# Performance work log

Hardware: AMD Instinct MI355X
Metric: run time of the kernel (lower is better)

## Reference

```python
import jax, jax.numpy as jnp
import numpy as np

HEADS = 16
DIM_HEAD = 64
DIM = 1024
SCALE = DIM_HEAD ** -0.5


def setup_inputs() -> dict:
    key = jax.random.key(0)
    ks = jax.random.split(key, 6)
    b, n = 1, 3072  # torch code is only shape-correct for b == 1

    def w(k, shape, fan_in):
        return jax.random.normal(k, shape, jnp.float32) * (fan_in ** -0.5)

    x = jax.random.normal(ks[0], (b, n, DIM), jnp.float32)
    Wqkv = w(ks[1], (DIM, 3 * HEADS * DIM_HEAD), DIM)          # to_qkv (no bias)
    W1 = w(ks[2], (DIM_HEAD, DIM_HEAD), DIM_HEAD)              # mlp layer 1
    b1 = jnp.zeros((DIM_HEAD,), jnp.float32)
    W2 = w(ks[3], (DIM_HEAD, 1), DIM_HEAD)                     # mlp layer 2
    b2 = jnp.zeros((1,), jnp.float32)
    Wout = w(ks[4], (HEADS * DIM_HEAD, DIM), HEADS * DIM_HEAD) # to_out
    bout = jnp.zeros((DIM,), jnp.float32)
    return {"x": x, "Wqkv": Wqkv, "W1": W1, "b1": b1, "W2": W2, "b2": b2,
            "Wout": Wout, "bout": bout}


def reference(x, Wqkv, W1, b1, W2, b2, Wout, bout):
    b, n, _ = x.shape
    qkv = x @ Wqkv                                   # [b, n, 3*h*d]
    q, k, v = jnp.split(qkv, 3, axis=-1)
    to_heads = lambda t: t.reshape(b, n, HEADS, DIM_HEAD).transpose(0, 2, 1, 3)
    q, k, v = to_heads(q), to_heads(k), to_heads(v)  # [b, h, n, d]

    dots = jnp.einsum('bhid,bhjd->bhij', q, k) * SCALE  # [b, h, n, n]

    # key spikiness MLP: Linear -> ReLU -> Linear -> Sigmoid, then softmax over n
    spiky = jax.nn.sigmoid(jnp.maximum(k @ W1 + b1, 0.0) @ W2 + b2)[..., 0]  # [b, h, n]
    spiky_weights = jax.nn.softmax(spiky, axis=-1)                            # [b, h, n]

    # For b=1 the torch broadcast reduces to a per-QUERY scaling of the logits
    weighted_dots = dots * spiky_weights[:, :, :, None]
    weights = jax.nn.softmax(weighted_dots, axis=-1)

    out = jnp.einsum('bhij,bhjd->bhid', weights, v)       # [b, h, n, d]
    out = out.transpose(0, 2, 1, 3).reshape(b, n, HEADS * DIM_HEAD)
    return out @ Wout + bout
```

## Files before the change

### kernel.cpp

```cpp
#include <hip/hip_runtime.h>
#include <hip/hip_bf16.h>
#include <math.h>

typedef __bf16 bf16_t;
typedef __bf16 bf16x8 __attribute__((ext_vector_type(8)));
typedef float floatx4 __attribute__((ext_vector_type(4)));

#define NSEQ 3072
#define QKVLD 3072
#define DMODEL 1024

__device__ inline bf16x8 load8(const float* p) {
    floatx4 a = *(const floatx4*)p;
    floatx4 b = *(const floatx4*)(p + 4);
    bf16x8 r;
    r[0] = (bf16_t)a[0]; r[1] = (bf16_t)a[1]; r[2] = (bf16_t)a[2]; r[3] = (bf16_t)a[3];
    r[4] = (bf16_t)b[0]; r[5] = (bf16_t)b[1]; r[6] = (bf16_t)b[2]; r[7] = (bf16_t)b[3];
    return r;
}

__device__ inline void gload16(const bf16_t* g, bf16_t* l) {
    __builtin_amdgcn_global_load_lds(
        (const __attribute__((address_space(1))) unsigned int*)g,
        (__attribute__((address_space(3))) unsigned int*)l, 16, 0, 0);
}

__global__ __launch_bounds__(256) void prep_kernel(const float* __restrict__ x,
                                                   const float* __restrict__ Wqkv,
                                                   const float* __restrict__ Wout,
                                                   bf16_t* __restrict__ xb,
                                                   bf16_t* __restrict__ WqkvT,
                                                   bf16_t* __restrict__ WoutT,
                                                   float* __restrict__ Mf) {
    __shared__ float T[64][65];
    const int b = blockIdx.x, tid = threadIdx.x;
    if (b < 1536) {
        int i = b * 2048 + tid * 8;
        *(bf16x8*)(xb + i) = load8(x + i);
        return;
    }
    if (b >= 2560) {
        const floatx4 z = {0.f, 0.f, 0.f, 0.f};
        if (b < 2576) {
            floatx4* p = (floatx4*)(Mf + (b - 2560) * 4096);
#pragma unroll
            for (int i = 0; i < 4; ++i) p[i * 256 + tid] = z;
        } else {
            float* zp = Mf + 65536;
            for (int i = tid; i < 2064; i += 256) zp[i] = 0.f;
        }
        return;
    }
    const float* in; bf16_t* out; int K, N, bx, by;
    if (b < 2304) { int l = b - 1536; bx = l % 48; by = l / 48; in = Wqkv; out = WqkvT; K = 1024; N = 3072; }
    else          { int l = b - 2304; bx = l & 15; by = l >> 4; in = Wout; out = WoutT; K = 1024; N = 1024; }
    const int n0 = bx * 64, k0 = by * 64;
    const int r = tid >> 2, c0 = (tid & 3) * 16;
#pragma unroll
    for (int i = 0; i < 4; ++i) {
        floatx4 v = *(const floatx4*)(in + (size_t)(k0 + r) * N + n0 + c0 + i * 4);
        T[r][c0 + i * 4 + 0] = v[0]; T[r][c0 + i * 4 + 1] = v[1];
        T[r][c0 + i * 4 + 2] = v[2]; T[r][c0 + i * 4 + 3] = v[3];
    }
    __syncthreads();
    bf16x8 o0, o1;
#pragma unroll
    for (int i = 0; i < 8; ++i) { o0[i] = (bf16_t)T[c0 + i][r]; o1[i] = (bf16_t)T[c0 + 8 + i][r]; }
    *(bf16x8*)(out + (size_t)(n0 + r) * K + k0 + c0)     = o0;
    *(bf16x8*)(out + (size_t)(n0 + r) * K + k0 + c0 + 8) = o1;
}

template <int TN, typename CT>
__global__ __launch_bounds__(256) void gemm_bt(const bf16_t* __restrict__ A,
                                               const bf16_t* __restrict__ BT,
                                               const float* __restrict__ bias,
                                               CT* __restrict__ C,
                                               int M, int N, int K) {
    constexpr int MI = (TN == 128) ? 4 : 2;
    __shared__ __attribute__((aligned(16))) bf16_t As[128 * 64];
    __shared__ __attribute__((aligned(16))) bf16_t Bs[TN * 64];
    const int tid = threadIdx.x;
    const int wave = tid >> 6, lane = tid & 63;
    const int lr = lane & 15, quad = lane >> 4;
    const int wr = (TN == 128) ? (wave >> 1) * 64 : wave * 32;
    const int wc = (TN == 128) ? (wave & 1) * 64 : 0;
    const int m0 = blockIdx.y * 128, n0 = blockIdx.x * TN;
    const int srow = lane >> 3;
    const int schunk = (lane & 7) ^ srow;

    const floatx4 fzero = {0.f, 0.f, 0.f, 0.f};
    floatx4 acc[MI][4];
#pragma unroll
    for (int mi = 0; mi < MI; ++mi)
#pragma unroll
        for (int ni = 0; ni < 4; ++ni) acc[mi][ni] = fzero;

    for (int kb = 0; kb < K; kb += 64) {
        __syncthreads();
#pragma unroll
        for (int it = 0; it < 4; ++it) {
            const int r0 = (wave * 4 + it) * 8;
            gload16(A + (size_t)(m0 + r0 + srow) * K + kb + schunk * 8, &As[r0 * 64]);
        }
#pragma unroll
        for (int it = 0; it < TN / 32; ++it) {
            const int r0 = (wave * (TN / 32) + it) * 8;
            gload16(BT + (size_t)(n0 + r0 + srow) * K + kb + schunk * 8, &Bs[r0 * 64]);
        }
        __syncthreads();
#pragma unroll
        for (int ch = 0; ch < 2; ++ch) {
            bf16x8 af[MI], bfr[4];
#pragma unroll
            for (int mi = 0; mi < MI; ++mi)
                af[mi] = *(const bf16x8*)(&As[(wr + mi * 16 + lr) * 64 + (((ch * 4 + quad) ^ (lr & 7)) * 8)]);
#pragma unroll
            for (int ni = 0; ni < 4; ++ni)
                bfr[ni] = *(const bf16x8*)(&Bs[(wc + ni * 16 + lr) * 64 + (((ch * 4 + quad) ^ (lr & 7)) * 8)]);
#pragma unroll
            for (int mi = 0; mi < MI; ++mi)
#pragma unroll
                for (int ni = 0; ni < 4; ++ni)
                    acc[mi][ni] = __builtin_amdgcn_mfma_f32_16x16x32_bf16(af[mi], bfr[ni], acc[mi][ni], 0, 0, 0);
        }
    }

#pragma unroll
    for (int mi = 0; mi < MI; ++mi)
#pragma unroll
        for (int ni = 0; ni < 4; ++ni) {
            int n = n0 + wc + ni * 16 + lr;
            float bv = bias ? bias[n] : 0.f;
#pragma unroll
            for (int r = 0; r < 4; ++r) {
                int m = m0 + wr + mi * 16 + quad * 4 + r;
                C[(size_t)m * N + n] = (CT)(acc[mi][ni][r] + bv);
            }
        }
}

__global__ __launch_bounds__(256) void prep2_kernel(const bf16_t* __restrict__ qkv,
                                                    const float* __restrict__ W1,
                                                    const float* __restrict__ b1,
                                                    const float* __restrict__ W2,
                                                    const float* __restrict__ b2,
                                                    float* __restrict__ sfull,
                                                    float* __restrict__ hsum,
                                                    float* __restrict__ Mf,
                                                    float* __restrict__ Ksumf,
                                                    float* __restrict__ Vsumf) {
    __shared__ __attribute__((aligned(16))) bf16_t Kt[64][72];
    __shared__ __attribute__((aligned(16))) bf16_t Vt[64][72];
    __shared__ float W1s[64][65];
    __shared__ float W2s[64], b1s[64];
    const int b = blockIdx.x, tid = threadIdx.x;
    if (b < 192) {
        const int h = b / 12, j = (b % 12) * 256 + tid;
        for (int i = tid; i < 4096; i += 256) W1s[i >> 6][i & 63] = W1[i];
        if (tid < 64) { W2s[tid] = W2[tid]; b1s[tid] = b1[tid]; }
        __syncthreads();
        float kv[64];
        const bf16x8* kp8 = (const bf16x8*)(qkv + (size_t)j * QKVLD + DMODEL + h * 64);
#pragma unroll
        for (int c = 0; c < 8; ++c) {
            bf16x8 v = kp8[c];
#pragma unroll
            for (int ii = 0; ii < 8; ++ii) kv[c * 8 + ii] = (float)v[ii];
        }
        float s = b2[0];
        for (int dd = 0; dd < 64; ++dd) {
            float a = b1s[dd];
#pragma unroll
            for (int d = 0; d < 64; ++d) a += kv[d] * W1s[d][dd];
            a = fmaxf(a, 0.f);
            s += a * W2s[dd];
        }
        s = 1.f / (1.f + __expf(-s));
        sfull[h * NSEQ + j] = s;
        float e = __expf(s);
#pragma unroll
        for (int off = 1; off < 64; off <<= 1) e += __shfl_xor(e, off, 64);
        if ((tid & 63) == 0) atomicAdd(&hsum[h], e);
    } else {
        const int l = b - 192;
        const int h = l / 12, c = l % 12;
        const int wave = tid >> 6, lane = tid & 63;
        const int lr = lane & 15, quad = lane >> 4;
        const int jj = tid >> 3, ch = (tid & 7) * 8;
        const floatx4 fzero = {0.f, 0.f, 0.f, 0.f};
        floatx4 macc[4];
#pragma unroll
        for (int ni = 0; ni < 4; ++ni) macc[ni] = fzero;
        float ksum = 0.f, vsum = 0.f;

        for (int st = 0; st < 4; ++st) {
            const size_t row0 = (size_t)(c * 256 + st * 64);
            bf16x8 k0 = *(const bf16x8*)(qkv + (row0 + jj) * QKVLD + DMODEL + h * 64 + ch);
            bf16x8 k1 = *(const bf16x8*)(qkv + (row0 + jj + 32) * QKVLD + DMODEL + h * 64 + ch);
            bf16x8 v0 = *(const bf16x8*)(qkv + (row0 + jj) * QKVLD + 2 * DMODEL + h * 64 + ch);
            bf16x8 v1 = *(const bf16x8*)(qkv + (row0 + jj + 32) * QKVLD + 2 * DMODEL + h * 64 + ch);
            __syncthreads();
#pragma unroll
            for (int ii = 0; ii < 8; ++ii) {
                Kt[ch + ii][jj] = k0[ii]; Kt[ch + ii][jj + 32] = k1[ii];
                Vt[ch + ii][jj] = v0[ii]; Vt[ch + ii][jj + 32] = v1[ii];
            }
            __syncthreads();
            bf16x8 a0 = *(const bf16x8*)(&Kt[wave * 16 + lr][quad * 8]);
            bf16x8 a1 = *(const bf16x8*)(&Kt[wave * 16 + lr][32 + quad * 8]);
#pragma unroll
            for (int ni = 0; ni < 4; ++ni) {
                bf16x8 b0 = *(const bf16x8*)(&Vt[ni * 16 + lr][quad * 8]);
                bf16x8 b1f = *(const bf16x8*)(&Vt[ni * 16 + lr][32 + quad * 8]);
                macc[ni] = __builtin_amdgcn_mfma_f32_16x16x32_bf16(a0, b0, macc[ni], 0, 0, 0);
                macc[ni] = __builtin_amdgcn_mfma_f32_16x16x32_bf16(a1, b1f, macc[ni], 0, 0, 0);
            }
            if (tid < 64) {
#pragma unroll
                for (int cc = 0; cc < 8; ++cc) {
                    bf16x8 kk = *(const bf16x8*)(&Kt[tid][cc * 8]);
#pragma unroll
                    for (int ii = 0; ii < 8; ++ii) ksum += (float)kk[ii];
                }
            } else if (tid < 128) {
                const int d = tid - 64;
#pragma unroll
                for (int cc = 0; cc < 8; ++cc) {
                    bf16x8 vv = *(const bf16x8*)(&Vt[d][cc * 8]);
#pragma unroll
                    for (int ii = 0; ii < 8; ++ii) vsum += (float)vv[ii];
                }
            }
        }
        float* mh = Mf + (size_t)h * 4096;
#pragma unroll
        for (int ni = 0; ni < 4; ++ni)
#pragma unroll
            for (int r = 0; r < 4; ++r)
                atomicAdd(&mh[(wave * 16 + quad * 4 + r) * 64 + ni * 16 + lr], macc[ni][r]);
        if (tid < 64) atomicAdd(&Ksumf[h * 64 + tid], ksum);
        else if (tid < 128) atomicAdd(&Vsumf[h * 64 + (tid - 64)], vsum);
    }
}

__global__ __launch_bounds__(256) void mid_kernel(const bf16_t* __restrict__ qkv,
                                                  const bf16_t* __restrict__ WoutT,
                                                  const float* __restrict__ Mf,
                                                  const float* __restrict__ Ksumf,
                                                  const float* __restrict__ Vsumf,
                                                  const float* __restrict__ sfull,
                                                  const float* __restrict__ hsum,
                                                  bf16_t* __restrict__ Gt,
                                                  bf16_t* __restrict__ Qt) {
    const int b = blockIdx.x, tid = threadIdx.x;
    if (b < 128) {
        __shared__ __attribute__((aligned(16))) bf16_t Ms[64][72];
        __shared__ float Vss[64];
        const int h = b >> 3, ot = b & 7;
        for (int i = tid; i < 4096; i += 256)
            Ms[i >> 6][i & 63] = (bf16_t)Mf[(size_t)h * 4096 + i];
        if (tid < 64) Vss[tid] = Vsumf[h * 64 + tid];
        __syncthreads();

        const int wave = tid >> 6, lane = tid & 63;
        const int lr = lane & 15, quad = lane >> 4;
        const floatx4 fzero = {0.f, 0.f, 0.f, 0.f};
        floatx4 acc[2][4];
#pragma unroll
        for (int mi = 0; mi < 2; ++mi)
#pragma unroll
            for (int ni = 0; ni < 4; ++ni) acc[mi][ni] = fzero;
#pragma unroll
        for (int chk = 0; chk < 2; ++chk) {
            bf16x8 af[2], bfr[4];
#pragma unroll
            for (int mi = 0; mi < 2; ++mi) {
                const int o = ot * 128 + wave * 32 + mi * 16 + lr;
                af[mi] = *(const bf16x8*)(WoutT + (size_t)o * 1024 + h * 64 + chk * 32 + quad * 8);
            }
#pragma unroll
            for (int ni = 0; ni < 4; ++ni)
                bfr[ni] = *(const bf16x8*)(&Ms[ni * 16 + lr][chk * 32 + quad * 8]);
#pragma unroll
            for (int mi = 0; mi < 2; ++mi)
#pragma unroll
                for (int ni = 0; ni < 4; ++ni)
                    acc[mi][ni] = __builtin_amdgcn_mfma_f32_16x16x32_bf16(af[mi], bfr[ni], acc[mi][ni], 0, 0, 0);
        }
#pragma unroll
        for (int mi = 0; mi < 2; ++mi)
#pragma unroll
            for (int ni = 0; ni < 4; ++ni)
#pragma unroll
                for (int r = 0; r < 4; ++r) {
                    const int o = ot * 128 + wave * 32 + mi * 16 + quad * 4 + r;
                    Gt[(size_t)o * 1088 + h * 64 + ni * 16 + lr] = (bf16_t)acc[mi][ni][r];
                }
        if (tid < 128) {
            const int o = ot * 128 + tid;
            float u = 0.f;
            const bf16x8* wp = (const bf16x8*)(WoutT + (size_t)o * 1024 + h * 64);
#pragma unroll
            for (int cc = 0; cc < 8; ++cc) {
                bf16x8 w = wp[cc];
#pragma unroll
                for (int ii = 0; ii < 8; ++ii) u += (float)w[ii] * Vss[cc * 8 + ii];
            }
            Gt[(size_t)o * 1088 + 1024 + h] = (bf16_t)u;
            if (h == 0) {
                const bf16x8 bz = {};
#pragma unroll
                for (int cc = 0; cc < 6; ++cc)
                    *(bf16x8*)(Gt + (size_t)o * 1088 + 1040 + cc * 8) = bz;
            }
        } else {
            const int o = ot * 128 + (tid - 128);
            float u = 0.f;
            const bf16x8* wp = (const bf16x8*)(WoutT + (size_t)o * 1024 + h * 64);
#pragma unroll
            for (int cc = 0; cc < 8; ++cc) {
                bf16x8 w = wp[cc];
#pragma unroll
                for (int ii = 0; ii < 8; ++ii) u += (float)w[ii] * Vss[cc * 8 + ii];
            }
            (void)u;
        }
    } else {
        __shared__ float Ks[1024];
        __shared__ float cinv[16];
        const int q0 = (b - 128) * 16;
        for (int i = tid; i < 1024; i += 256) Ks[i] = Ksumf[i];
        if (tid < 16) cinv[tid] = 0.125f / hsum[tid];
        __syncthreads();
        const int q = q0 + (tid >> 4), h = tid & 15;
        const bf16x8* qp = (const bf16x8*)(qkv + (size_t)q * QKVLD + h * 64);
        bf16x8 qv[8];
        float dot = 0.f;
#pragma unroll
        for (int cc = 0; cc < 8; ++cc) {
            qv[cc] = qp[cc];
#pragma unroll
            for (int ii = 0; ii < 8; ++ii) dot += (float)qv[cc][ii] * Ks[h * 64 + cc * 8 + ii];
        }
        const float c = __expf(sfull[h * NSEQ + q]) * cinv[h];
        const float den = (float)NSEQ + c * dot;
        const float w = c / den;
#pragma unroll
        for (int cc = 0; cc < 8; ++cc) {
            bf16x8 o;
#pragma unroll
            for (int ii = 0; ii < 8; ++ii) o[ii] = (bf16_t)(w * (float)qv[cc][ii]);
            *(bf16x8*)(Qt + (size_t)q * 1088 + h * 64 + cc * 8) = o;
        }
        Qt[(size_t)q * 1088 + 1024 + h] = (bf16_t)(1.f / den);
        if (h < 6) {
            const bf16x8 bz = {};
            *(bf16x8*)(Qt + (size_t)q * 1088 + 1040 + h * 8) = bz;
        }
    }
}

extern "C" void kernel_launch(void* const* d_in, const int* in_sizes, int n_in,
                              void* d_out, int out_size, void* d_ws, size_t ws_size,
                              hipStream_t stream) {
    const float* x    = (const float*)d_in[0];
    const float* Wqkv = (const float*)d_in[1];
    const float* W1   = (const float*)d_in[2];
    const float* b1   = (const float*)d_in[3];
    const float* W2   = (const float*)d_in[4];
    const float* b2   = (const float*)d_in[5];
    const float* Wout = (const float*)d_in[6];
    const float* bout = (const float*)d_in[7];
    float* out = (float*)d_out;

    char* ws = (char*)d_ws;
    bf16_t* WqkvT = (bf16_t*)(ws);
    bf16_t* WoutT = (bf16_t*)(ws + 6291456);
    bf16_t* qkv   = (bf16_t*)(ws + 8388608);
    bf16_t* xb    = (bf16_t*)(ws + 27262976);
    bf16_t* Qt    = (bf16_t*)(ws + 33554432);
    bf16_t* Gt    = (bf16_t*)(ws + 40239104);
    float*  Mf    = (float*)(ws + 42467328);
    float*  Ksumf = (float*)(ws + 42729472);
    float*  Vsumf = (float*)(ws + 42733568);
    float*  hsum  = (float*)(ws + 42737664);
    float*  sfull = (float*)(ws + 42737728);

    prep_kernel<<<2577, 256, 0, stream>>>(x, Wqkv, Wout, xb, WqkvT, WoutT, Mf);
    gemm_bt<128, bf16_t><<<dim3(24, 24), 256, 0, stream>>>(xb, WqkvT, nullptr, qkv, NSEQ, NSEQ, DMODEL);
    prep2_kernel<<<384, 256, 0, stream>>>(qkv, W1, b1, W2, b2, sfull, hsum, Mf, Ksumf, Vsumf);
    mid_kernel<<<320, 256, 0, stream>>>(qkv, WoutT, Mf, Ksumf, Vsumf, sfull, hsum, Gt, Qt);
    gemm_bt<64, float><<<dim3(16, 24), 256, 0, stream>>>(Qt, Gt, bout, out, NSEQ, DMODEL, 1088);
}
```

Before: 181.6 us.

## Compute key spikiness MLP with MFMA using a pre-transposed bf16 W1

The per-key MLP in prep2 was a scalar FP32 loop in which each thread did 64x64 FMAs against W1 held in LDS. It now runs as bf16 MFMA 16x16x32 tiles per wave, followed by ReLU, a dot with W2 done through lane shuffles, and the sigmoid. W1 is transposed and cast to bf16 in an extra prep block, which lowers the precision of the first layer. The change also drops a dead branch in mid_kernel that computed and discarded a dot product.

```diff
diff --git a/kernel.cpp b/kernel.cpp
--- a/kernel.cpp
+++ b/kernel.cpp
@@ -28,9 +28,11 @@
 __global__ __launch_bounds__(256) void prep_kernel(const float* __restrict__ x,
                                                    const float* __restrict__ Wqkv,
                                                    const float* __restrict__ Wout,
+                                                   const float* __restrict__ W1,
                                                    bf16_t* __restrict__ xb,
                                                    bf16_t* __restrict__ WqkvT,
                                                    bf16_t* __restrict__ WoutT,
+                                                   bf16_t* __restrict__ W1T,
                                                    float* __restrict__ Mf) {
     __shared__ float T[64][65];
     const int b = blockIdx.x, tid = threadIdx.x;
@@ -45,9 +47,14 @@
             floatx4* p = (floatx4*)(Mf + (b - 2560) * 4096);
 #pragma unroll
             for (int i = 0; i < 4; ++i) p[i * 256 + tid] = z;
-        } else {
+        } else if (b == 2576) {
             float* zp = Mf + 65536;
             for (int i = tid; i < 2064; i += 256) zp[i] = 0.f;
+        } else {
+            for (int i = tid; i < 4096; i += 256) {
+                const int dd = i >> 6, d = i & 63;
+                W1T[i] = (bf16_t)W1[d * 64 + dd];
+            }
         }
         return;
     }
@@ -140,7 +147,7 @@
 }
 
 __global__ __launch_bounds__(256) void prep2_kernel(const bf16_t* __restrict__ qkv,
-                                                    const float* __restrict__ W1,
+                                                    const bf16_t* __restrict__ W1T,
                                                     const float* __restrict__ b1,
                                                     const float* __restrict__ W2,
                                                     const float* __restrict__ b2,
@@ -149,43 +156,63 @@
                                                     float* __restrict__ Mf,
                                                     float* __restrict__ Ksumf,
                                                     float* __restrict__ Vsumf) {
-    __shared__ __attribute__((aligned(16))) bf16_t Kt[64][72];
-    __shared__ __attribute__((aligned(16))) bf16_t Vt[64][72];
-    __shared__ float W1s[64][65];
-    __shared__ float W2s[64], b1s[64];
     const int b = blockIdx.x, tid = threadIdx.x;
+    const int wave = tid >> 6, lane = tid & 63;
+    const int lr = lane & 15, quad = lane >> 4;
     if (b < 192) {
-        const int h = b / 12, j = (b % 12) * 256 + tid;
-        for (int i = tid; i < 4096; i += 256) W1s[i >> 6][i & 63] = W1[i];
-        if (tid < 64) { W2s[tid] = W2[tid]; b1s[tid] = b1[tid]; }
-        __syncthreads();
-        float kv[64];
-        const bf16x8* kp8 = (const bf16x8*)(qkv + (size_t)j * QKVLD + DMODEL + h * 64);
-#pragma unroll
-        for (int c = 0; c < 8; ++c) {
-            bf16x8 v = kp8[c];
-#pragma unroll
-            for (int ii = 0; ii < 8; ++ii) kv[c * 8 + ii] = (float)v[ii];
-        }
-        float s = b2[0];
-        for (int dd = 0; dd < 64; ++dd) {
-            float a = b1s[dd];
-#pragma unroll
-            for (int d = 0; d < 64; ++d) a += kv[d] * W1s[d][dd];
-            a = fmaxf(a, 0.f);
-            s += a * W2s[dd];
-        }
-        s = 1.f / (1.f + __expf(-s));
-        sfull[h * NSEQ + j] = s;
-        float e = __expf(s);
-#pragma unroll
-        for (int off = 1; off < 64; off <<= 1) e += __shfl_xor(e, off, 64);
-        if ((tid & 63) == 0) atomicAdd(&hsum[h], e);
+        const int h = b / 12;
+        const int jbase = (b % 12) * 256 + wave * 64;
+        const bf16_t* kb = qkv + DMODEL + h * 64;
+        const floatx4 fzero = {0.f, 0.f, 0.f, 0.f};
+        floatx4 acc[4][4];
+#pragma unroll
+        for (int mi = 0; mi < 4; ++mi)
+#pragma unroll
+            for (int ni = 0; ni < 4; ++ni) acc[mi][ni] = fzero;
+#pragma unroll
+        for (int ch = 0; ch < 2; ++ch) {
+            bf16x8 af[4], bfr[4];
+#pragma unroll
+            for (int mi = 0; mi < 4; ++mi)
+                af[mi] = *(const bf16x8*)(kb + (size_t)(jbase + mi * 16 + lr) * QKVLD + ch * 32 + quad * 8);
+#pragma unroll
+            for (int ni = 0; ni < 4; ++ni)
+                bfr[ni] = *(const bf16x8*)(W1T + (ni * 16 + lr) * 64 + ch * 32 + quad * 8);
+#pragma unroll
+            for (int mi = 0; mi < 4; ++mi)
+#pragma unroll
+                for (int ni = 0; ni < 4; ++ni)
+                    acc[mi][ni] = __builtin_amdgcn_mfma_f32_16x16x32_bf16(af[mi], bfr[ni], acc[mi][ni], 0, 0, 0);
+        }
+        float b1v[4], W2v[4];
+#pragma unroll
+        for (int ni = 0; ni < 4; ++ni) { b1v[ni] = b1[ni * 16 + lr]; W2v[ni] = W2[ni * 16 + lr]; }
+        const float b2v = b2[0];
+        float eh = 0.f;
+#pragma unroll
+        for (int mi = 0; mi < 4; ++mi)
+#pragma unroll
+            for (int r = 0; r < 4; ++r) {
+                float p = 0.f;
+#pragma unroll
+                for (int ni = 0; ni < 4; ++ni)
+                    p += fmaxf(acc[mi][ni][r] + b1v[ni], 0.f) * W2v[ni];
+#pragma unroll
+                for (int off = 1; off < 16; off <<= 1) p += __shfl_xor(p, off, 64);
+                const float s = 1.f / (1.f + __expf(-(b2v + p)));
+                if (lr == 0) {
+                    sfull[h * NSEQ + jbase + mi * 16 + quad * 4 + r] = s;
+                    eh += __expf(s);
+                }
+            }
+        eh += __shfl_xor(eh, 16, 64);
+        eh += __shfl_xor(eh, 32, 64);
+        if (lane == 0) atomicAdd(&hsum[h], eh);
     } else {
+        __shared__ __attribute__((aligned(16))) bf16_t Kt[64][72];
+        __shared__ __attribute__((aligned(16))) bf16_t Vt[64][72];
         const int l = b - 192;
         const int h = l / 12, c = l % 12;
-        const int wave = tid >> 6, lane = tid & 63;
-        const int lr = lane & 15, quad = lane >> 4;
         const int jj = tid >> 3, ch = (tid & 7) * 8;
         const floatx4 fzero = {0.f, 0.f, 0.f, 0.f};
         floatx4 macc[4];
@@ -313,17 +340,6 @@
                 for (int cc = 0; cc < 6; ++cc)
                     *(bf16x8*)(Gt + (size_t)o * 1088 + 1040 + cc * 8) = bz;
             }
-        } else {
-            const int o = ot * 128 + (tid - 128);
-            float u = 0.f;
-            const bf16x8* wp = (const bf16x8*)(WoutT + (size_t)o * 1024 + h * 64);
-#pragma unroll
-            for (int cc = 0; cc < 8; ++cc) {
-                bf16x8 w = wp[cc];
-#pragma unroll
-                for (int ii = 0; ii < 8; ++ii) u += (float)w[ii] * Vss[cc * 8 + ii];
-            }
-            (void)u;
         }
     } else {
         __shared__ float Ks[1024];
@@ -385,10 +401,11 @@
     float*  Vsumf = (float*)(ws + 42733568);
     float*  hsum  = (float*)(ws + 42737664);
     float*  sfull = (float*)(ws + 42737728);
-
-    prep_kernel<<<2577, 256, 0, stream>>>(x, Wqkv, Wout, xb, WqkvT, WoutT, Mf);
+    bf16_t* W1T   = (bf16_t*)(ws + 42934336);
+
+    prep_kernel<<<2578, 256, 0, stream>>>(x, Wqkv, Wout, W1, xb, WqkvT, WoutT, W1T, Mf);
     gemm_bt<128, bf16_t><<<dim3(24, 24), 256, 0, stream>>>(xb, WqkvT, nullptr, qkv, NSEQ, NSEQ, DMODEL);
-    prep2_kernel<<<384, 256, 0, stream>>>(qkv, W1, b1, W2, b2, sfull, hsum, Mf, Ksumf, Vsumf);
+    prep2_kernel<<<384, 256, 0, stream>>>(qkv, W1T, b1, W2, b2, sfull, hsum, Mf, Ksumf, Vsumf);
     mid_kernel<<<320, 256, 0, stream>>>(qkv, WoutT, Mf, Ksumf, Vsumf, sfull, hsum, Gt, Qt);
     gemm_bt<64, float><<<dim3(16, 24), 256, 0, stream>>>(Qt, Gt, bout, out, NSEQ, DMODEL, 1088);
 }
```

After: 161.2 us. 11.2% less time.
